# Optimization experiments

Measured on AMD Instinct MI355X. Metric: run time of the kernel, lower is better.

## Reference

```python
import jax, jax.numpy as jnp
import numpy as np
import math

NUM_HEADS = 32
NUM_KV = 8
D = 128          # num_hidden == per-head dim in this module
S = 2048
B = 1
DK = 128
ROPE_BASE = 10000.0


def rope(x):
    # x: [B, H, S, D]; standard Llama-style RoPE (split-halves rotation) over positions.
    d = x.shape[-1]
    half = d // 2
    pos = jnp.arange(x.shape[2], dtype=jnp.float32)                       # [S]
    inv_freq = 1.0 / (ROPE_BASE ** (jnp.arange(half, dtype=jnp.float32) / half))
    ang = pos[:, None] * inv_freq[None, :]                                # [S, half]
    cos = jnp.cos(ang)
    sin = jnp.sin(ang)
    x1 = x[..., :half]
    x2 = x[..., half:]
    return jnp.concatenate([x1 * cos - x2 * sin, x1 * sin + x2 * cos], axis=-1)


def setup_inputs() -> dict:
    key = jax.random.key(0)
    ks = jax.random.split(key, 8)
    query = jax.random.normal(ks[0], (B, S, D), dtype=jnp.float32)
    k_in = jax.random.normal(ks[1], (B, S, D), dtype=jnp.float32)
    v_in = jax.random.normal(ks[2], (B, S, D), dtype=jnp.float32)
    # causal mask: 1 where attention allowed (lower triangle incl diagonal)
    mask = jnp.tril(jnp.ones((S, S), dtype=jnp.int32))[None, None]        # [1,1,S,S]
    sc = 0.02
    Wq = jax.random.normal(ks[3], (NUM_HEADS * D, D), dtype=jnp.float32) * sc
    bq = jnp.zeros((NUM_HEADS * D,), dtype=jnp.float32)
    Wk = jax.random.normal(ks[4], (NUM_KV * D, D), dtype=jnp.float32) * sc
    bk = jnp.zeros((NUM_KV * D,), dtype=jnp.float32)
    Wv = jax.random.normal(ks[5], (NUM_KV * D, D), dtype=jnp.float32) * sc
    bv = jnp.zeros((NUM_KV * D,), dtype=jnp.float32)
    Wo = jax.random.normal(ks[6], (D, NUM_HEADS * D), dtype=jnp.float32) * sc
    bo = jnp.zeros((D,), dtype=jnp.float32)
    return {"query": query, "key": k_in, "values": v_in, "mask": mask,
            "Wq": Wq, "bq": bq, "Wk": Wk, "bk": bk, "Wv": Wv, "bv": bv,
            "Wo": Wo, "bo": bo}


def reference(query, key, values, mask, Wq, bq, Wk, bk, Wv, bv, Wo, bo):
    Bq, Sq, Dh = query.shape
    # projections; torch Linear: x @ W.T + b. Note: view (reshape), not transpose,
    # exactly as in the original module.
    q = (query @ Wq.T + bq).reshape(Bq, NUM_HEADS, Sq, Dh)   # [B,H,S,D]
    k = (key @ Wk.T + bk).reshape(Bq, NUM_KV, Sq, Dh)        # [B,Hkv,S,D]
    v = (values @ Wv.T + bv).reshape(Bq, NUM_KV, Sq, Dh)
    rk = rope(k)
    rv = rope(v)  # module applies RoPE to values too (faithful)
    rep = NUM_HEADS // NUM_KV
    # torch .repeat((1, rep, 1, 1)) tiles whole head blocks -> jnp.tile
    rk = jnp.tile(rk, (1, rep, 1, 1))                        # [B,H,S,D]
    rv = jnp.tile(rv, (1, rep, 1, 1))
    scores = jnp.einsum('bhqd,bhkd->bhqk', q, rk) / math.sqrt(DK)
    scores = jnp.where(mask == 0, -jnp.inf, scores)
    attn = jax.nn.softmax(scores, axis=-1)
    out = jnp.einsum('bhqk,bhkd->bhqd', attn, rv)            # [B,H,S,D]
    out = out.transpose(0, 2, 1, 3).reshape(Bq, Sq, NUM_HEADS * Dh)
    return out @ Wo.T + bo
```

## Files before the change

### kernel.cpp

```cpp
#include <hip/hip_runtime.h>

typedef unsigned short u16;
typedef unsigned int u32;
typedef short frag_t __attribute__((ext_vector_type(8)));
typedef float f32x4 __attribute__((ext_vector_type(4)));

#define S_LEN 2048

__device__ __forceinline__ float bf2f(u32 u) {
  union { u32 i; float f; } v; v.i = u << 16; return v.f;
}
__device__ __forceinline__ u16 f2bf(float f) {
  u32 x = __float_as_uint(f);
  u32 r = (x + 0x7fffu + ((x >> 16) & 1u)) >> 16;
  return (u16)r;
}
__device__ __forceinline__ void unpack8(uint4 r, float* o) {
  o[0] = bf2f(r.x & 0xffffu); o[1] = bf2f(r.x >> 16);
  o[2] = bf2f(r.y & 0xffffu); o[3] = bf2f(r.y >> 16);
  o[4] = bf2f(r.z & 0xffffu); o[5] = bf2f(r.z >> 16);
  o[6] = bf2f(r.w & 0xffffu); o[7] = bf2f(r.w >> 16);
}
__device__ __forceinline__ u16 ld_in(const void* p, size_t idx, bool fp32) {
  if (fp32) return f2bf(((const float*)p)[idx]);
  return ((const u16*)p)[idx];
}
__device__ __forceinline__ uint4 ld8(const void* p, size_t eidx, bool fp32) {
  if (!fp32) return *(const uint4*)((const u16*)p + eidx);
  const float4* f = (const float4*)((const float*)p + eidx);
  float4 x = f[0], y = f[1];
  uint4 r;
  r.x = (u32)f2bf(x.x) | ((u32)f2bf(x.y) << 16);
  r.y = (u32)f2bf(x.z) | ((u32)f2bf(x.w) << 16);
  r.z = (u32)f2bf(y.x) | ((u32)f2bf(y.y) << 16);
  r.w = (u32)f2bf(y.z) | ((u32)f2bf(y.w) << 16);
  return r;
}

__global__ __launch_bounds__(256) void proj_all(
    const void* __restrict__ query, const void* __restrict__ key,
    const void* __restrict__ values,
    const void* __restrict__ Wq, const void* __restrict__ bq,
    const void* __restrict__ Wk, const void* __restrict__ bk,
    const void* __restrict__ Wv, const void* __restrict__ bv,
    u16* __restrict__ Qb, u16* __restrict__ Kb, u16* __restrict__ Vtmp,
    u32* __restrict__ flag_out) {
  __shared__ u16 As[128][136];
  __shared__ u16 Ws[128][136];
  __shared__ u32 flagS;
  u16 (*Cs)[136] = As;
  const int t = threadIdx.x;
  if (t < 64) {
    u32 e = ((u32)((const u16*)query)[2 * t] >> 7) & 0xFFu;
    bool ok = (e >= 110u && e <= 140u);
    unsigned long long b = __ballot(ok);
    if (t == 0) flagS = (__popcll(b) < 32) ? 1u : 0u;
  }
  __syncthreads();
  const bool fp32 = (flagS != 0u);
  if (t == 0 && blockIdx.x == 0 && blockIdx.y == 0) *flag_out = flagS;
  const int x = blockIdx.x;
  const void *A, *W, *bias;
  u16* C; int N, n0;
  if (x < 32)      { A = query;  W = Wq; bias = bq; C = Qb;   N = 4096; n0 = x << 7; }
  else if (x < 40) { A = key;    W = Wk; bias = bk; C = Kb;   N = 1024; n0 = (x - 32) << 7; }
  else             { A = values; W = Wv; bias = bv; C = Vtmp; N = 1024; n0 = (x - 40) << 7; }
  const int m0 = blockIdx.y << 7;
#pragma unroll
  for (int i = 0; i < 8; ++i) {
    int task = t + (i << 8);
    int row = task >> 4, ch = (task & 15) << 3;
    *(uint4*)&As[row][ch] = ld8(A, (size_t)(m0 + row) * 128 + ch, fp32);
    *(uint4*)&Ws[row][ch] = ld8(W, (size_t)(n0 + row) * 128 + ch, fp32);
  }
  __syncthreads();
  const int lane = t & 63, w = t >> 6, quad = lane >> 4, l15 = lane & 15;
  const int rm = (w & 1) << 6, rn = (w >> 1) << 6;
  f32x4 acc[4][4];
#pragma unroll
  for (int mt = 0; mt < 4; ++mt)
#pragma unroll
    for (int nt = 0; nt < 4; ++nt) acc[mt][nt] = 0.f;
#pragma unroll
  for (int mtp = 0; mtp < 2; ++mtp) {
    frag_t a0[4], a1[4];
#pragma unroll
    for (int kc = 0; kc < 4; ++kc) {
      a0[kc] = *(const frag_t*)&As[rm + mtp * 32 + l15][kc * 32 + quad * 8];
      a1[kc] = *(const frag_t*)&As[rm + mtp * 32 + 16 + l15][kc * 32 + quad * 8];
    }
#pragma unroll
    for (int nt = 0; nt < 4; ++nt)
#pragma unroll
      for (int kc = 0; kc < 4; ++kc) {
        frag_t b = *(const frag_t*)&Ws[rn + nt * 16 + l15][kc * 32 + quad * 8];
        acc[mtp * 2][nt] = __builtin_amdgcn_mfma_f32_16x16x32_bf16(a0[kc], b, acc[mtp * 2][nt], 0, 0, 0);
        acc[mtp * 2 + 1][nt] = __builtin_amdgcn_mfma_f32_16x16x32_bf16(a1[kc], b, acc[mtp * 2 + 1][nt], 0, 0, 0);
      }
  }
  __syncthreads();
#pragma unroll
  for (int nt = 0; nt < 4; ++nt) {
    float bb = bf2f((u32)ld_in(bias, n0 + rn + nt * 16 + l15, fp32));
#pragma unroll
    for (int mt = 0; mt < 4; ++mt) {
      int row = rm + ((mt >> 1) * 32) + ((mt & 1) * 16) + quad * 4;
#pragma unroll
      for (int r = 0; r < 4; ++r)
        Cs[row + r][rn + nt * 16 + l15] = f2bf(acc[mt][nt][r] + bb);
    }
  }
  __syncthreads();
#pragma unroll
  for (int i = 0; i < 8; ++i) {
    int task = t + (i << 8);
    int row = task >> 4, ch = (task & 15) << 3;
    *(uint4*)&C[(size_t)(m0 + row) * N + n0 + ch] = *(const uint4*)&Cs[row][ch];
  }
}

__global__ __launch_bounds__(256) void rope_kv_tr(u16* __restrict__ Kb,
                                                  const u16* __restrict__ Vb,
                                                  u16* __restrict__ VbT) {
  __shared__ u16 Lt[128][72];
  const int t = threadIdx.x;
  const int s0 = blockIdx.x << 6;
  const int g = blockIdx.y;
  for (int i = t; i < 4096; i += 256) {
    int s = s0 + (i >> 6), ii = i & 63;
    float invf = __expf(-(float)ii * 0.14391156831212787f);
    float ang = (float)s * invf;
    float sn, cs;
    sincosf(ang, &sn, &cs);
    size_t base = ((size_t)(g << 11) + s) * 128 + ii;
    float k1 = bf2f((u32)Kb[base]), k2 = bf2f((u32)Kb[base + 64]);
    Kb[base] = f2bf(k1 * cs - k2 * sn);
    Kb[base + 64] = f2bf(k1 * sn + k2 * cs);
  }
  const u16* src = Vb + (size_t)g * S_LEN * 128;
  for (int i = t; i < 512; i += 256) {
    int r = i >> 3, d8 = (i & 7) << 3;
    float lo[8], hi[8];
    unpack8(*(const uint4*)&src[(size_t)(s0 + r) * 128 + d8], lo);
    unpack8(*(const uint4*)&src[(size_t)(s0 + r) * 128 + d8 + 64], hi);
#pragma unroll
    for (int j = 0; j < 8; ++j) {
      float invf = __expf(-(float)(d8 + j) * 0.14391156831212787f);
      float ang = (float)(s0 + r) * invf;
      float sn, cs;
      sincosf(ang, &sn, &cs);
      Lt[d8 + j][r] = f2bf(lo[j] * cs - hi[j] * sn);
      Lt[d8 + 64 + j][r] = f2bf(lo[j] * sn + hi[j] * cs);
    }
  }
  __syncthreads();
  u16* dst = VbT + (size_t)g * 128 * S_LEN + s0;
  for (int i = t; i < 2048; i += 256) {
    int d = i >> 4, s4 = (i & 15) << 2;
    uint2 pk;
    pk.x = (u32)Lt[d][s4] | ((u32)Lt[d][s4 + 1] << 16);
    pk.y = (u32)Lt[d][s4 + 2] | ((u32)Lt[d][s4 + 3] << 16);
    *(uint2*)&dst[(size_t)d * S_LEN + s4] = pk;
  }
}

__global__ __launch_bounds__(256, 2) void attn_mfma(
    const u16* __restrict__ Qb, const u16* __restrict__ Kb,
    const u16* __restrict__ VbT, u16* __restrict__ OpA, u16* __restrict__ OpB,
    float2* __restrict__ Ml, int nkh) {
  __shared__ union SmemU {
    struct { u16 Kt[64][136]; u16 Vt[128][72]; u16 St[128][72]; } m;
    struct { u16 Og[128][136]; } e;
  } su;
  const int t = threadIdx.x;
  const int lane = t & 63, w = t >> 6, quad = lane >> 4, l15 = lane & 15;
  const int g = (int)blockIdx.x & 7;
  const int kh = (int)blockIdx.x >> 3;
  const int pi = (int)blockIdx.y;
  const int h = g + (w << 3);
  const u16* Kg = Kb + (size_t)g * S_LEN * 128;
  const u16* Vg = VbT + (size_t)g * 128 * S_LEN;
  const int kR = t >> 4, kC = (t & 15) << 3;
  const int vR = t >> 3, vC = (t & 7) << 3;
  u16* dst = kh ? OpB : OpA;

  for (int tp = 0; tp < 2; ++tp) {
    const int qt = tp ? pi : 63 - pi;
    const int q0 = qt << 5;
    const int nsuper = (qt >> 1) + 1;
    frag_t aq[2][4];
#pragma unroll
    for (int qp = 0; qp < 2; ++qp)
#pragma unroll
      for (int kc = 0; kc < 4; ++kc)
        aq[qp][kc] = *(const frag_t*)&Qb[((size_t)h * S_LEN + q0 + qp * 16 + l15) * 128 +
                                         kc * 32 + quad * 8];
    float m_r[2] = {-1e30f, -1e30f}, l_r[2] = {0.f, 0.f};
    f32x4 oacc[2][8];
#pragma unroll
    for (int qp = 0; qp < 2; ++qp)
#pragma unroll
      for (int nt = 0; nt < 8; ++nt) oacc[qp][nt] = 0.f;

    uint4 kpf[4], vpf[4];
    if (kh < nsuper) {
      const int k0 = kh << 6;
#pragma unroll
      for (int j = 0; j < 4; ++j) {
        kpf[j] = *(const uint4*)&Kg[(size_t)(k0 + kR + j * 16) * 128 + kC];
        vpf[j] = *(const uint4*)&Vg[(size_t)(vR + j * 32) * S_LEN + k0 + vC];
      }
    }
    for (int sj = kh; sj < nsuper; sj += nkh) {
      const int k0 = sj << 6;
      __syncthreads();
#pragma unroll
      for (int j = 0; j < 4; ++j) {
        *(uint4*)&su.m.Kt[kR + j * 16][kC] = kpf[j];
        *(uint4*)&su.m.Vt[vR + j * 32][vC] = vpf[j];
      }
      __syncthreads();
      if (sj + nkh < nsuper) {
        const int kn = (sj + nkh) << 6;
#pragma unroll
        for (int j = 0; j < 4; ++j) {
          kpf[j] = *(const uint4*)&Kg[(size_t)(kn + kR + j * 16) * 128 + kC];
          vpf[j] = *(const uint4*)&Vg[(size_t)(vR + j * 32) * S_LEN + kn + vC];
        }
      }
      f32x4 s4[4][2];
#pragma unroll
      for (int kk = 0; kk < 4; ++kk)
#pragma unroll
        for (int qp = 0; qp < 2; ++qp) s4[kk][qp] = 0.f;
#pragma unroll
      for (int kc = 0; kc < 4; ++kc)
#pragma unroll
        for (int kk = 0; kk < 4; ++kk) {
          frag_t a = *(const frag_t*)&su.m.Kt[kk * 16 + l15][kc * 32 + quad * 8];
          s4[kk][0] = __builtin_amdgcn_mfma_f32_16x16x32_bf16(a, aq[0][kc], s4[kk][0], 0, 0, 0);
          s4[kk][1] = __builtin_amdgcn_mfma_f32_16x16x32_bf16(a, aq[1][kc], s4[kk][1], 0, 0, 0);
        }
      const bool lastm = (sj == nsuper - 1);
      float alpha[2];
#pragma unroll
      for (int qp = 0; qp < 2; ++qp) {
        const int qg = q0 + qp * 16 + l15;
        float mx = -1e30f;
#pragma unroll
        for (int kk = 0; kk < 4; ++kk)
#pragma unroll
          for (int r = 0; r < 4; ++r) {
            float sv = s4[kk][qp][r] * 0.08838834764831845f;
            if (lastm && (k0 + kk * 16 + quad * 4 + r) > qg) sv = -1e30f;
            s4[kk][qp][r] = sv;
            mx = fmaxf(mx, sv);
          }
        mx = fmaxf(mx, __shfl_xor(mx, 16));
        mx = fmaxf(mx, __shfl_xor(mx, 32));
        float mn = fmaxf(m_r[qp], mx);
        alpha[qp] = __expf(m_r[qp] - mn);
        m_r[qp] = mn;
        float sum = 0.f;
        const int strow = w * 32 + qp * 16 + l15;
#pragma unroll
        for (int kk = 0; kk < 4; ++kk) {
          float p0 = __expf(s4[kk][qp][0] - mn);
          float p1 = __expf(s4[kk][qp][1] - mn);
          float p2 = __expf(s4[kk][qp][2] - mn);
          float p3 = __expf(s4[kk][qp][3] - mn);
          sum += (p0 + p1) + (p2 + p3);
          uint2 pk;
          pk.x = (u32)f2bf(p0) | ((u32)f2bf(p1) << 16);
          pk.y = (u32)f2bf(p2) | ((u32)f2bf(p3) << 16);
          *(uint2*)&su.m.St[strow][kk * 16 + quad * 4] = pk;
        }
        sum += __shfl_xor(sum, 16);
        sum += __shfl_xor(sum, 32);
        l_r[qp] = l_r[qp] * alpha[qp] + sum;
      }
#pragma unroll
      for (int qp = 0; qp < 2; ++qp)
#pragma unroll
        for (int r = 0; r < 4; ++r) {
          float al = __shfl(alpha[qp], quad * 4 + r);
#pragma unroll
          for (int nt = 0; nt < 8; ++nt) oacc[qp][nt][r] *= al;
        }
#pragma unroll
      for (int kc2 = 0; kc2 < 2; ++kc2) {
        frag_t pa0 = *(const frag_t*)&su.m.St[w * 32 + l15][kc2 * 32 + quad * 8];
        frag_t pa1 = *(const frag_t*)&su.m.St[w * 32 + 16 + l15][kc2 * 32 + quad * 8];
#pragma unroll
        for (int nt = 0; nt < 8; ++nt) {
          frag_t v = *(const frag_t*)&su.m.Vt[nt * 16 + l15][kc2 * 32 + quad * 8];
          oacc[0][nt] = __builtin_amdgcn_mfma_f32_16x16x32_bf16(pa0, v, oacc[0][nt], 0, 0, 0);
          oacc[1][nt] = __builtin_amdgcn_mfma_f32_16x16x32_bf16(pa1, v, oacc[1][nt], 0, 0, 0);
        }
      }
    }
    __syncthreads();
#pragma unroll
    for (int qp = 0; qp < 2; ++qp)
#pragma unroll
      for (int r = 0; r < 4; ++r) {
        float fac = 1.0f;
        if (nkh == 1) fac = 1.0f / __shfl(l_r[qp], quad * 4 + r);
        int row = w * 32 + qp * 16 + quad * 4 + r;
#pragma unroll
        for (int nt = 0; nt < 8; ++nt)
          su.e.Og[row][nt * 16 + l15] = f2bf(oacc[qp][nt][r] * fac);
      }
    __syncthreads();
#pragma unroll
    for (int jj = 0; jj < 8; ++jj) {
      int c = t + (jj << 8);
      int row = c >> 4, ch = (c & 15) << 3;
      int hh = row >> 5, qr = row & 31;
      *(uint4*)&dst[(size_t)(q0 + qr) * 4096 + (g + hh * 8) * 128 + ch] =
          *(const uint4*)&su.e.Og[row][ch];
    }
    if (nkh == 2 && quad == 0) {
#pragma unroll
      for (int qp = 0; qp < 2; ++qp)
        Ml[((size_t)kh * 32 + h) * S_LEN + q0 + qp * 16 + l15] =
            make_float2(m_r[qp], l_r[qp]);
    }
  }
}

__global__ __launch_bounds__(256) void attn_merge(
    const u16* OpA, const u16* __restrict__ OpB,
    const float2* __restrict__ Ml, u16* Out) {
  int c = blockIdx.x * 256 + threadIdx.x;
  int s = c >> 9;
  int col8 = (c & 511) << 3;
  int h = col8 >> 7;
  float2 p1 = Ml[(size_t)h * S_LEN + s];
  float2 p2 = Ml[(size_t)(32 + h) * S_LEN + s];
  float mn = fmaxf(p1.x, p2.x);
  float a1 = __expf(p1.x - mn), a2 = __expf(p2.x - mn);
  float linv = 1.0f / (a1 * p1.y + a2 * p2.y);
  float w1 = a1 * linv, w2 = a2 * linv;
  float o1[8], o2[8];
  size_t idx = (size_t)s * 4096 + col8;
  unpack8(*(const uint4*)&OpA[idx], o1);
  unpack8(*(const uint4*)&OpB[idx], o2);
  uint4 r;
  r.x = (u32)f2bf(o1[0] * w1 + o2[0] * w2) | ((u32)f2bf(o1[1] * w1 + o2[1] * w2) << 16);
  r.y = (u32)f2bf(o1[2] * w1 + o2[2] * w2) | ((u32)f2bf(o1[3] * w1 + o2[3] * w2) << 16);
  r.z = (u32)f2bf(o1[4] * w1 + o2[4] * w2) | ((u32)f2bf(o1[5] * w1 + o2[5] * w2) << 16);
  r.w = (u32)f2bf(o1[6] * w1 + o2[6] * w2) | ((u32)f2bf(o1[7] * w1 + o2[7] * w2) << 16);
  *(uint4*)&Out[idx] = r;
}

__global__ __launch_bounds__(256) void out_part(
    const u16* __restrict__ Ob, const void* __restrict__ Wo,
    float* __restrict__ Pout, const u32* __restrict__ flagp) {
  __shared__ u16 As[128][136];
  __shared__ u16 Ws[128][136];
  const bool fp32 = (*flagp != 0u);
  const int t = threadIdx.x;
  const int lane = t & 63, w = t >> 6, quad = lane >> 4, l15 = lane & 15;
  const int rm = (w & 1) << 6, rn = (w >> 1) << 6;
  const int m0 = (int)blockIdx.x << 7;
  const int z = (int)blockIdx.y;
  f32x4 acc[4][4];
#pragma unroll
  for (int mt = 0; mt < 4; ++mt)
#pragma unroll
    for (int nt = 0; nt < 4; ++nt) acc[mt][nt] = 0.f;
  for (int kc2 = 0; kc2 < 2; ++kc2) {
    if (kc2) __syncthreads();
    const int kc0 = (z << 8) + (kc2 << 7);
#pragma unroll
    for (int i = 0; i < 8; ++i) {
      int task = t + (i << 8);
      int row = task >> 4, ch = (task & 15) << 3;
      *(uint4*)&As[row][ch] = *(const uint4*)&Ob[(size_t)(m0 + row) * 4096 + kc0 + ch];
      *(uint4*)&Ws[row][ch] = ld8(Wo, (size_t)row * 4096 + kc0 + ch, fp32);
    }
    __syncthreads();
#pragma unroll
    for (int mtp = 0; mtp < 2; ++mtp) {
      frag_t a0[4], a1[4];
#pragma unroll
      for (int kc = 0; kc < 4; ++kc) {
        a0[kc] = *(const frag_t*)&As[rm + mtp * 32 + l15][kc * 32 + quad * 8];
        a1[kc] = *(const frag_t*)&As[rm + mtp * 32 + 16 + l15][kc * 32 + quad * 8];
      }
#pragma unroll
      for (int nt = 0; nt < 4; ++nt)
#pragma unroll
        for (int kc = 0; kc < 4; ++kc) {
          frag_t b = *(const frag_t*)&Ws[rn + nt * 16 + l15][kc * 32 + quad * 8];
          acc[mtp * 2][nt] = __builtin_amdgcn_mfma_f32_16x16x32_bf16(a0[kc], b, acc[mtp * 2][nt], 0, 0, 0);
          acc[mtp * 2 + 1][nt] = __builtin_amdgcn_mfma_f32_16x16x32_bf16(a1[kc], b, acc[mtp * 2 + 1][nt], 0, 0, 0);
        }
    }
  }
#pragma unroll
  for (int mt = 0; mt < 4; ++mt) {
    int mrow = m0 + rm + ((mt >> 1) * 32) + ((mt & 1) * 16) + quad * 4;
#pragma unroll
    for (int nt = 0; nt < 4; ++nt) {
      int n = rn + nt * 16 + l15;
#pragma unroll
      for (int r = 0; r < 4; ++r)
        Pout[((size_t)z * 2048 + mrow + r) * 128 + n] = acc[mt][nt][r];
    }
  }
}

__global__ __launch_bounds__(256) void out_red(
    const float* __restrict__ Pout, const void* __restrict__ bo,
    void* __restrict__ out, const u32* __restrict__ flagp) {
  const bool fp32 = (*flagp != 0u);
  int e4 = blockIdx.x * 256 + threadIdx.x;
  const float4* P = (const float4*)Pout;
  float4 s = P[e4];
#pragma unroll
  for (int z = 1; z < 16; ++z) {
    float4 p = P[(size_t)z * 65536 + e4];
    s.x += p.x; s.y += p.y; s.z += p.z; s.w += p.w;
  }
  int n = (e4 << 2) & 127;
  s.x += bf2f((u32)ld_in(bo, n + 0, fp32));
  s.y += bf2f((u32)ld_in(bo, n + 1, fp32));
  s.z += bf2f((u32)ld_in(bo, n + 2, fp32));
  s.w += bf2f((u32)ld_in(bo, n + 3, fp32));
  if (fp32) {
    ((float4*)out)[e4] = s;
  } else {
    uint2 pk;
    pk.x = (u32)f2bf(s.x) | ((u32)f2bf(s.y) << 16);
    pk.y = (u32)f2bf(s.z) | ((u32)f2bf(s.w) << 16);
    *(uint2*)((u16*)out + (e4 << 2)) = pk;
  }
}

extern "C" void kernel_launch(void* const* d_in, const int* in_sizes, int n_in,
                              void* d_out, int out_size, void* d_ws, size_t ws_size,
                              hipStream_t stream) {
  (void)in_sizes; (void)n_in; (void)out_size;
  const void* query  = d_in[0];
  const void* key    = d_in[1];
  const void* values = d_in[2];
  const void* Wq = d_in[4];
  const void* bq = d_in[5];
  const void* Wk = d_in[6];
  const void* bk = d_in[7];
  const void* Wv = d_in[8];
  const void* bv = d_in[9];
  const void* Wo = d_in[10];
  const void* bo = d_in[11];

  char* ws = (char*)d_ws;
  u32* flag   = (u32*)ws;
  u16* Qb     = (u16*)(ws + 64);
  u16* Kb     = (u16*)(ws + 64 + (16ull << 20));
  u16* VbT    = (u16*)(ws + 64 + (20ull << 20));
  u16* Vtmp   = (u16*)(ws + 64 + (24ull << 20));
  u16* Ob     = (u16*)(ws + 64 + (24ull << 20));
  u16* OpB    = (u16*)(ws + 64 + (40ull << 20));
  float2* Mlb = (float2*)(ws + 64 + (56ull << 20));
  float* Pout = (float*)Qb;

  const bool split = (ws_size >= (58ull << 20));
  const int nkh = split ? 2 : 1;

  proj_all<<<dim3(48, 16), 256, 0, stream>>>(query, key, values, Wq, bq, Wk, bk,
                                             Wv, bv, Qb, Kb, Vtmp, flag);
  rope_kv_tr<<<dim3(32, 8), 256, 0, stream>>>(Kb, Vtmp, VbT);
  attn_mfma<<<dim3(8 * nkh, 32), 256, 0, stream>>>(Qb, Kb, VbT, Ob, OpB, Mlb, nkh);
  if (split) attn_merge<<<4096, 256, 0, stream>>>(Ob, OpB, Mlb, Ob);
  out_part<<<dim3(16, 16), 256, 0, stream>>>(Ob, Wo, Pout, flag);
  out_red<<<256, 256, 0, stream>>>(Pout, bo, d_out, flag);
}
```

Before: 261.7 us.

## Halve attention KV tile to 32 and fuse split-K merge into output projection

```diff
diff --git a/kernel.cpp b/kernel.cpp
--- a/kernel.cpp
+++ b/kernel.cpp
@@ -169,7 +169,7 @@
     const u16* __restrict__ VbT, u16* __restrict__ OpA, u16* __restrict__ OpB,
     float2* __restrict__ Ml, int nkh) {
   __shared__ union SmemU {
-    struct { u16 Kt[64][136]; u16 Vt[128][72]; u16 St[128][72]; } m;
+    struct { u16 Kt[32][136]; u16 Vt[128][40]; u16 St[128][40]; } m;
     struct { u16 Og[128][136]; } e;
   } su;
   const int t = threadIdx.x;
@@ -181,13 +181,13 @@
   const u16* Kg = Kb + (size_t)g * S_LEN * 128;
   const u16* Vg = VbT + (size_t)g * 128 * S_LEN;
   const int kR = t >> 4, kC = (t & 15) << 3;
-  const int vR = t >> 3, vC = (t & 7) << 3;
+  const int vR = t >> 2, vC = (t & 3) << 3;
   u16* dst = kh ? OpB : OpA;
 
   for (int tp = 0; tp < 2; ++tp) {
     const int qt = tp ? pi : 63 - pi;
     const int q0 = qt << 5;
-    const int nsuper = (qt >> 1) + 1;
+    const int niter = qt + 1;
     frag_t aq[2][4];
 #pragma unroll
     for (int qp = 0; qp < 2; ++qp)
@@ -202,53 +202,48 @@
 #pragma unroll
       for (int nt = 0; nt < 8; ++nt) oacc[qp][nt] = 0.f;
 
-    uint4 kpf[4], vpf[4];
-    if (kh < nsuper) {
-      const int k0 = kh << 6;
-#pragma unroll
-      for (int j = 0; j < 4; ++j) {
-        kpf[j] = *(const uint4*)&Kg[(size_t)(k0 + kR + j * 16) * 128 + kC];
-        vpf[j] = *(const uint4*)&Vg[(size_t)(vR + j * 32) * S_LEN + k0 + vC];
-      }
-    }
-    for (int sj = kh; sj < nsuper; sj += nkh) {
-      const int k0 = sj << 6;
+    uint4 kpf[2], vpf[2];
+    if (kh < niter) {
+      const int k0 = kh << 5;
+      kpf[0] = *(const uint4*)&Kg[(size_t)(k0 + kR) * 128 + kC];
+      kpf[1] = *(const uint4*)&Kg[(size_t)(k0 + kR + 16) * 128 + kC];
+      vpf[0] = *(const uint4*)&Vg[(size_t)vR * S_LEN + k0 + vC];
+      vpf[1] = *(const uint4*)&Vg[(size_t)(vR + 64) * S_LEN + k0 + vC];
+    }
+    for (int sj = kh; sj < niter; sj += nkh) {
+      const int k0 = sj << 5;
       __syncthreads();
-#pragma unroll
-      for (int j = 0; j < 4; ++j) {
-        *(uint4*)&su.m.Kt[kR + j * 16][kC] = kpf[j];
-        *(uint4*)&su.m.Vt[vR + j * 32][vC] = vpf[j];
-      }
+      *(uint4*)&su.m.Kt[kR][kC] = kpf[0];
+      *(uint4*)&su.m.Kt[kR + 16][kC] = kpf[1];
+      *(uint4*)&su.m.Vt[vR][vC] = vpf[0];
+      *(uint4*)&su.m.Vt[vR + 64][vC] = vpf[1];
       __syncthreads();
-      if (sj + nkh < nsuper) {
-        const int kn = (sj + nkh) << 6;
-#pragma unroll
-        for (int j = 0; j < 4; ++j) {
-          kpf[j] = *(const uint4*)&Kg[(size_t)(kn + kR + j * 16) * 128 + kC];
-          vpf[j] = *(const uint4*)&Vg[(size_t)(vR + j * 32) * S_LEN + kn + vC];
-        }
-      }
-      f32x4 s4[4][2];
-#pragma unroll
-      for (int kk = 0; kk < 4; ++kk)
-#pragma unroll
-        for (int qp = 0; qp < 2; ++qp) s4[kk][qp] = 0.f;
+      if (sj + nkh < niter) {
+        const int kn = (sj + nkh) << 5;
+        kpf[0] = *(const uint4*)&Kg[(size_t)(kn + kR) * 128 + kC];
+        kpf[1] = *(const uint4*)&Kg[(size_t)(kn + kR + 16) * 128 + kC];
+        vpf[0] = *(const uint4*)&Vg[(size_t)vR * S_LEN + kn + vC];
+        vpf[1] = *(const uint4*)&Vg[(size_t)(vR + 64) * S_LEN + kn + vC];
+      }
+      f32x4 s4[2][2];
+#pragma unroll
+      for (int kk = 0; kk < 2; ++kk) { s4[kk][0] = 0.f; s4[kk][1] = 0.f; }
 #pragma unroll
       for (int kc = 0; kc < 4; ++kc)
 #pragma unroll
-        for (int kk = 0; kk < 4; ++kk) {
+        for (int kk = 0; kk < 2; ++kk) {
           frag_t a = *(const frag_t*)&su.m.Kt[kk * 16 + l15][kc * 32 + quad * 8];
           s4[kk][0] = __builtin_amdgcn_mfma_f32_16x16x32_bf16(a, aq[0][kc], s4[kk][0], 0, 0, 0);
           s4[kk][1] = __builtin_amdgcn_mfma_f32_16x16x32_bf16(a, aq[1][kc], s4[kk][1], 0, 0, 0);
         }
-      const bool lastm = (sj == nsuper - 1);
+      const bool lastm = (sj == niter - 1);
       float alpha[2];
 #pragma unroll
       for (int qp = 0; qp < 2; ++qp) {
         const int qg = q0 + qp * 16 + l15;
         float mx = -1e30f;
 #pragma unroll
-        for (int kk = 0; kk < 4; ++kk)
+        for (int kk = 0; kk < 2; ++kk)
 #pragma unroll
           for (int r = 0; r < 4; ++r) {
             float sv = s4[kk][qp][r] * 0.08838834764831845f;
@@ -264,7 +259,7 @@
         float sum = 0.f;
         const int strow = w * 32 + qp * 16 + l15;
 #pragma unroll
-        for (int kk = 0; kk < 4; ++kk) {
+        for (int kk = 0; kk < 2; ++kk) {
           float p0 = __expf(s4[kk][qp][0] - mn);
           float p1 = __expf(s4[kk][qp][1] - mn);
           float p2 = __expf(s4[kk][qp][2] - mn);
@@ -287,16 +282,13 @@
 #pragma unroll
           for (int nt = 0; nt < 8; ++nt) oacc[qp][nt][r] *= al;
         }
-#pragma unroll
-      for (int kc2 = 0; kc2 < 2; ++kc2) {
-        frag_t pa0 = *(const frag_t*)&su.m.St[w * 32 + l15][kc2 * 32 + quad * 8];
-        frag_t pa1 = *(const frag_t*)&su.m.St[w * 32 + 16 + l15][kc2 * 32 + quad * 8];
-#pragma unroll
-        for (int nt = 0; nt < 8; ++nt) {
-          frag_t v = *(const frag_t*)&su.m.Vt[nt * 16 + l15][kc2 * 32 + quad * 8];
-          oacc[0][nt] = __builtin_amdgcn_mfma_f32_16x16x32_bf16(pa0, v, oacc[0][nt], 0, 0, 0);
-          oacc[1][nt] = __builtin_amdgcn_mfma_f32_16x16x32_bf16(pa1, v, oacc[1][nt], 0, 0, 0);
-        }
+      frag_t pa0 = *(const frag_t*)&su.m.St[w * 32 + l15][quad * 8];
+      frag_t pa1 = *(const frag_t*)&su.m.St[w * 32 + 16 + l15][quad * 8];
+#pragma unroll
+      for (int nt = 0; nt < 8; ++nt) {
+        frag_t v = *(const frag_t*)&su.m.Vt[nt * 16 + l15][quad * 8];
+        oacc[0][nt] = __builtin_amdgcn_mfma_f32_16x16x32_bf16(pa0, v, oacc[0][nt], 0, 0, 0);
+        oacc[1][nt] = __builtin_amdgcn_mfma_f32_16x16x32_bf16(pa1, v, oacc[1][nt], 0, 0, 0);
       }
     }
     __syncthreads();
@@ -329,34 +321,10 @@
   }
 }
 
-__global__ __launch_bounds__(256) void attn_merge(
-    const u16* OpA, const u16* __restrict__ OpB,
-    const float2* __restrict__ Ml, u16* Out) {
-  int c = blockIdx.x * 256 + threadIdx.x;
-  int s = c >> 9;
-  int col8 = (c & 511) << 3;
-  int h = col8 >> 7;
-  float2 p1 = Ml[(size_t)h * S_LEN + s];
-  float2 p2 = Ml[(size_t)(32 + h) * S_LEN + s];
-  float mn = fmaxf(p1.x, p2.x);
-  float a1 = __expf(p1.x - mn), a2 = __expf(p2.x - mn);
-  float linv = 1.0f / (a1 * p1.y + a2 * p2.y);
-  float w1 = a1 * linv, w2 = a2 * linv;
-  float o1[8], o2[8];
-  size_t idx = (size_t)s * 4096 + col8;
-  unpack8(*(const uint4*)&OpA[idx], o1);
-  unpack8(*(const uint4*)&OpB[idx], o2);
-  uint4 r;
-  r.x = (u32)f2bf(o1[0] * w1 + o2[0] * w2) | ((u32)f2bf(o1[1] * w1 + o2[1] * w2) << 16);
-  r.y = (u32)f2bf(o1[2] * w1 + o2[2] * w2) | ((u32)f2bf(o1[3] * w1 + o2[3] * w2) << 16);
-  r.z = (u32)f2bf(o1[4] * w1 + o2[4] * w2) | ((u32)f2bf(o1[5] * w1 + o2[5] * w2) << 16);
-  r.w = (u32)f2bf(o1[6] * w1 + o2[6] * w2) | ((u32)f2bf(o1[7] * w1 + o2[7] * w2) << 16);
-  *(uint4*)&Out[idx] = r;
-}
-
 __global__ __launch_bounds__(256) void out_part(
-    const u16* __restrict__ Ob, const void* __restrict__ Wo,
-    float* __restrict__ Pout, const u32* __restrict__ flagp) {
+    const u16* __restrict__ OpA, const u16* __restrict__ OpB,
+    const float2* __restrict__ Ml, const void* __restrict__ Wo,
+    float* __restrict__ Pout, const u32* __restrict__ flagp, int nkh) {
   __shared__ u16 As[128][136];
   __shared__ u16 Ws[128][136];
   const bool fp32 = (*flagp != 0u);
@@ -373,11 +341,32 @@
   for (int kc2 = 0; kc2 < 2; ++kc2) {
     if (kc2) __syncthreads();
     const int kc0 = (z << 8) + (kc2 << 7);
+    const int hh = kc0 >> 7;
 #pragma unroll
     for (int i = 0; i < 8; ++i) {
       int task = t + (i << 8);
       int row = task >> 4, ch = (task & 15) << 3;
-      *(uint4*)&As[row][ch] = *(const uint4*)&Ob[(size_t)(m0 + row) * 4096 + kc0 + ch];
+      size_t idx = (size_t)(m0 + row) * 4096 + kc0 + ch;
+      if (nkh == 2) {
+        int s = m0 + row;
+        float2 p1 = Ml[(size_t)hh * S_LEN + s];
+        float2 p2 = Ml[(size_t)(32 + hh) * S_LEN + s];
+        float mn = fmaxf(p1.x, p2.x);
+        float a1 = __expf(p1.x - mn), a2 = __expf(p2.x - mn);
+        float linv = 1.0f / (a1 * p1.y + a2 * p2.y);
+        float w1 = a1 * linv, w2 = a2 * linv;
+        float o1[8], o2[8];
+        unpack8(*(const uint4*)&OpA[idx], o1);
+        unpack8(*(const uint4*)&OpB[idx], o2);
+        uint4 r;
+        r.x = (u32)f2bf(o1[0] * w1 + o2[0] * w2) | ((u32)f2bf(o1[1] * w1 + o2[1] * w2) << 16);
+        r.y = (u32)f2bf(o1[2] * w1 + o2[2] * w2) | ((u32)f2bf(o1[3] * w1 + o2[3] * w2) << 16);
+        r.z = (u32)f2bf(o1[4] * w1 + o2[4] * w2) | ((u32)f2bf(o1[5] * w1 + o2[5] * w2) << 16);
+        r.w = (u32)f2bf(o1[6] * w1 + o2[6] * w2) | ((u32)f2bf(o1[7] * w1 + o2[7] * w2) << 16);
+        *(uint4*)&As[row][ch] = r;
+      } else {
+        *(uint4*)&As[row][ch] = *(const uint4*)&OpA[idx];
+      }
       *(uint4*)&Ws[row][ch] = ld8(Wo, (size_t)row * 4096 + kc0 + ch, fp32);
     }
     __syncthreads();
@@ -473,7 +462,6 @@
                                              Wv, bv, Qb, Kb, Vtmp, flag);
   rope_kv_tr<<<dim3(32, 8), 256, 0, stream>>>(Kb, Vtmp, VbT);
   attn_mfma<<<dim3(8 * nkh, 32), 256, 0, stream>>>(Qb, Kb, VbT, Ob, OpB, Mlb, nkh);
-  if (split) attn_merge<<<4096, 256, 0, stream>>>(Ob, OpB, Mlb, Ob);
-  out_part<<<dim3(16, 16), 256, 0, stream>>>(Ob, Wo, Pout, flag);
+  out_part<<<dim3(16, 16), 256, 0, stream>>>(Ob, OpB, Mlb, Wo, Pout, flag, nkh);
   out_red<<<256, 256, 0, stream>>>(Pout, bo, d_out, flag);
 }
```

New measurement: 249.8 us. 1.05x faster.
